# Kernel tuning notes

Measured on AMD Instinct MI355X. Metric: run time of the kernel, lower is better.

Reference implementation:

```python
import jax, jax.numpy as jnp
import numpy as np

D, H, DFF, DC = 1024, 16, 4096, 768
DH = D // H
EPS = 1e-5

def layer_norm(x, g, b):
    m = jnp.mean(x, axis=-1, keepdims=True)
    v = jnp.mean(jnp.square(x - m), axis=-1, keepdims=True)
    return (x - m) * jax.lax.rsqrt(v + EPS) * g + b

def setup_inputs() -> dict:
    key = jax.random.key(0)
    ks = jax.random.split(key, 20)
    s = 0.02
    return {
        "x": jax.random.normal(ks[0], (2, 2048, D), jnp.float32),
        "cond": jax.random.normal(ks[1], (2, 77, DC), jnp.float32),
        # self-attention params
        "Wqkv": jax.random.normal(ks[2], (D, 3 * D), jnp.float32) * s,
        "Wproj_sa": jax.random.normal(ks[3], (D, D), jnp.float32) * s,
        "bproj_sa": jnp.zeros((D,), jnp.float32),
        "g1": jnp.ones((D,), jnp.float32),
        "b1": jnp.zeros((D,), jnp.float32),
        # cross-attention params
        "Wq_ca": jax.random.normal(ks[4], (D, D), jnp.float32) * s,
        "Wkv_ca": jax.random.normal(ks[5], (DC, 2 * D), jnp.float32) * s,
        "Wproj_ca": jax.random.normal(ks[6], (D, D), jnp.float32) * s,
        "bproj_ca": jnp.zeros((D,), jnp.float32),
        "g2": jnp.ones((D,), jnp.float32),
        "b2": jnp.zeros((D,), jnp.float32),
        # feed-forward params
        "Wff1": jax.random.normal(ks[7], (D, DFF), jnp.float32) * s,
        "bff1": jnp.zeros((DFF,), jnp.float32),
        "Wff2": jax.random.normal(ks[8], (DFF, D), jnp.float32) * s,
        "bff2": jnp.zeros((D,), jnp.float32),
        "g3": jnp.ones((D,), jnp.float32),
        "b3": jnp.zeros((D,), jnp.float32),
    }

def _self_attn(x, Wqkv, Wproj, bproj):
    B, T, _ = x.shape
    qkv = x @ Wqkv                                   # (B,T,3D)
    qkv = qkv.reshape(B, T, 3, H, DH)
    q, k, v = (qkv[:, :, i].transpose(0, 2, 1, 3) for i in range(3))  # (B,H,T,DH)
    scale = DH ** -0.5
    attn = jnp.einsum('bhtd,bhsd->bhts', q, k) * scale  # (B,H,T,T)
    causal = jnp.triu(jnp.ones((T, T), bool), k=1)
    attn = jnp.where(causal, -jnp.inf, attn)
    attn = jax.nn.softmax(attn, axis=-1)
    out = jnp.einsum('bhts,bhsd->bhtd', attn, v)
    out = out.transpose(0, 2, 1, 3).reshape(B, T, D)
    return out @ Wproj + bproj

def _cross_attn(x, cond, Wq, Wkv, Wproj, bproj):
    B, T, _ = x.shape
    C = cond.shape[1]
    q = (x @ Wq).reshape(B, T, H, DH).transpose(0, 2, 1, 3)      # (B,H,T,DH)
    kv = (cond @ Wkv).reshape(B, C, 2, H, DH)
    k = kv[:, :, 0].transpose(0, 2, 1, 3)                         # (B,H,C,DH)
    v = kv[:, :, 1].transpose(0, 2, 1, 3)
    scale = DH ** -0.5
    attn = jax.nn.softmax(jnp.einsum('bhtd,bhcd->bhtc', q, k) * scale, axis=-1)
    out = jnp.einsum('bhtc,bhcd->bhtd', attn, v)
    out = out.transpose(0, 2, 1, 3).reshape(B, T, D)
    return out @ Wproj + bproj

def reference(x, cond, Wqkv, Wproj_sa, bproj_sa, g1, b1,
              Wq_ca, Wkv_ca, Wproj_ca, bproj_ca, g2, b2,
              Wff1, bff1, Wff2, bff2, g3, b3):
    x = x + _self_attn(layer_norm(x, g1, b1), Wqkv, Wproj_sa, bproj_sa)
    x = x + _cross_attn(layer_norm(x, g2, b2), cond, Wq_ca, Wkv_ca, Wproj_ca, bproj_ca)
    h = layer_norm(x, g3, b3)
    h = jax.nn.gelu(h @ Wff1 + bff1, approximate=False) @ Wff2 + bff2
    return x + h
```

## Files before the change

kernel.cpp:

```cpp
#include <hip/hip_runtime.h>

using bf16   = __bf16;
using bf16x8 = __attribute__((ext_vector_type(8))) bf16;
using bf16x4 = __attribute__((ext_vector_type(4))) bf16;
using f32x4  = __attribute__((ext_vector_type(4))) float;

#define DEV static __device__ __forceinline__

DEV void MFMA16(bf16x8 a, bf16x8 b, f32x4& c){
  c = __builtin_amdgcn_mfma_f32_16x16x32_bf16(a, b, c, 0, 0, 0);
}

DEV void gload16(const bf16* g, bf16* lds){
  __builtin_amdgcn_global_load_lds(
      (const __attribute__((address_space(1))) void*)g,
      (__attribute__((address_space(3))) void*)lds, 16, 0, 0);
}

DEV void tcast4_dev(const float* __restrict__ in, bf16* __restrict__ out,
                    int R, int C, int bx, int by, float scale, int nscale,
                    int tid, float (*t)[129])
{
  const int c0 = bx*128, r0 = by*32;
  #pragma unroll
  for (int i = 0; i < 4; ++i){
    int row = i*8 + (tid >> 5);
    int col = (tid & 31) * 4;
    const float4 v = *(const float4*)&in[(size_t)(r0+row)*C + c0 + col];
    t[row][col+0]=v.x; t[row][col+1]=v.y; t[row][col+2]=v.z; t[row][col+3]=v.w;
  }
  __syncthreads();
  const int c = tid >> 1, rh = (tid & 1) * 16;
  const float sc = (c0 + c < nscale) ? scale : 1.f;
  bf16 tmp[16];
  #pragma unroll
  for (int j = 0; j < 16; ++j) tmp[j] = (bf16)(t[rh+j][c] * sc);
  bf16* o = out + (size_t)(c0+c)*R + r0 + rh;
  *(bf16x8*)o       = *(bf16x8*)&tmp[0];
  *(bf16x8*)(o + 8) = *(bf16x8*)&tmp[8];
}

DEV void ln_dev(const float* __restrict__ x, const float* __restrict__ gw,
                const float* __restrict__ bw, bf16* __restrict__ y,
                int row, int tid, float (*red)[4])
{
  const float4 v = ((const float4*)(x + (size_t)row*1024))[tid];
  float s  = v.x+v.y+v.z+v.w;
  float s2 = v.x*v.x+v.y*v.y+v.z*v.z+v.w*v.w;
  #pragma unroll
  for (int off=32; off>=1; off>>=1){ s += __shfl_down(s,off); s2 += __shfl_down(s2,off); }
  const int wid = tid>>6, lane = tid&63;
  if (lane==0){ red[0][wid]=s; red[1][wid]=s2; }
  __syncthreads();
  s  = red[0][0]+red[0][1]+red[0][2]+red[0][3];
  s2 = red[1][0]+red[1][1]+red[1][2]+red[1][3];
  const float m  = s*(1.f/1024.f);
  const float rs = rsqrtf(s2*(1.f/1024.f) - m*m + 1e-5f);
  const float4 gv = ((const float4*)gw)[tid];
  const float4 bv = ((const float4*)bw)[tid];
  bf16* yr = y + (size_t)row*1024 + tid*4;
  yr[0] = (bf16)((v.x-m)*rs*gv.x + bv.x);
  yr[1] = (bf16)((v.y-m)*rs*gv.y + bv.y);
  yr[2] = (bf16)((v.z-m)*rs*gv.z + bv.z);
  yr[3] = (bf16)((v.w-m)*rs*gv.w + bv.w);
}

__global__ __launch_bounds__(256) void prep_ln(
    const float* Wqkv, bf16* wqkvT, const float* Wps, bf16* wpsT,
    const float* Wqc, bf16* wqcT, const float* Wkvc, bf16* wkvcT,
    const float* Wpc, bf16* wpcT, const float* Wf1, bf16* wf1T,
    const float* Wf2, bf16* wf2T, const float* cond, bf16* condb,
    const float* x, const float* g1, const float* b1, bf16* xn)
{
  __shared__ float t[32][129];
  __shared__ float red[2][4];
  const int bid = blockIdx.x, tid = threadIdx.x;
  if      (bid <  768) tcast4_dev(Wqkv, wqkvT, 1024, 3072, bid%24,        bid/24,        0.125f, 1024, tid, t);
  else if (bid < 1024) tcast4_dev(Wps,  wpsT,  1024, 1024, (bid-768)%8,   (bid-768)/8,   1.f, 0, tid, t);
  else if (bid < 1280) tcast4_dev(Wqc,  wqcT,  1024, 1024, (bid-1024)%8,  (bid-1024)/8,  0.125f, 1024, tid, t);
  else if (bid < 1664) tcast4_dev(Wkvc, wkvcT,  768, 2048, (bid-1280)%16, (bid-1280)/16, 1.f, 0, tid, t);
  else if (bid < 1920) tcast4_dev(Wpc,  wpcT,  1024, 1024, (bid-1664)%8,  (bid-1664)/8,  1.f, 0, tid, t);
  else if (bid < 2944) tcast4_dev(Wf1,  wf1T,  1024, 4096, (bid-1920)%32, (bid-1920)/32, 1.f, 0, tid, t);
  else if (bid < 3968) tcast4_dev(Wf2,  wf2T,  4096, 1024, (bid-2944)%8,  (bid-2944)/8,  1.f, 0, tid, t);
  else if (bid < 4084) {
    int i = (bid-3968)*256 + tid;
    if (i < 29568) {
      const float4 v = ((const float4*)cond)[i];
      bf16 o[4] = {(bf16)v.x,(bf16)v.y,(bf16)v.z,(bf16)v.w};
      *(bf16x4*)&condb[i*4] = *(bf16x4*)o;
    }
  } else {
    ln_dev(x, g1, b1, xn, bid - 4084, tid, red);
  }
}

__global__ __launch_bounds__(256) void ln_kernel(const float* __restrict__ x,
    const float* __restrict__ gw, const float* __restrict__ bw, bf16* __restrict__ y)
{
  __shared__ float red[2][4];
  ln_dev(x, gw, bw, y, blockIdx.x, threadIdx.x, red);
}

__global__ __launch_bounds__(256) void ln_re(
    const float* __restrict__ x1, const float* __restrict__ g2,
    const float* __restrict__ b2, bf16* __restrict__ xn,
    const bf16* __restrict__ kvca, bf16* __restrict__ kpad, bf16* __restrict__ vtca)
{
  __shared__ float red[2][4];
  const int bid = blockIdx.x, tid = threadIdx.x;
  if (bid < 4096) {
    ln_dev(x1, g2, b2, xn, bid, tid, red);
  } else {
    int idx = (bid - 4096)*256 + tid;
    int d = idx & 63, s = (idx>>6) & 127, h = (idx>>13) & 15, b = idx>>17;
    bf16 kv = (bf16)0.f, vv = (bf16)0.f;
    if (s < 77) {
      kv = kvca[(size_t)(b*77+s)*2048 + h*64 + d];
      vv = kvca[(size_t)(b*77+s)*2048 + 1024 + h*64 + d];
    }
    kpad[idx] = kv;
    vtca[(((size_t)(b*16+h)*64 + d)<<7) + s] = vv;
  }
}

template<int MODE>
__global__ __launch_bounds__(512) void gemm256p(
    const bf16* __restrict__ A, const bf16* __restrict__ Bt,
    const float* __restrict__ bias, const float* resid,
    void* outp, int M, int N, int K)
{
  __shared__ __align__(16) bf16 As[2][256*64];
  __shared__ __align__(16) bf16 Bs[2][256*64];
  const int tid = threadIdx.x;
  const int lane = tid & 63, wid = tid >> 6;
  const int l15 = lane & 15, lh = lane >> 4;
  const int wm = wid >> 2, wn = wid & 3;

  const int nwg = gridDim.x * gridDim.y;
  const int lin = blockIdx.y * gridDim.x + blockIdx.x;
  const int wg  = (lin & 7) * (nwg >> 3) + (lin >> 3);
  const size_t m0 = (size_t)(wg / gridDim.x) * 256;
  const size_t n0 = (size_t)(wg % gridDim.x) * 256;

  f32x4 acc[8][4];
  #pragma unroll
  for (int i=0;i<8;++i)
    #pragma unroll
    for (int j=0;j<4;++j) acc[i][j] = (f32x4){0.f,0.f,0.f,0.f};

  const int srow8 = lane >> 3;
  const int scol  = ((lane & 7) ^ srow8) * 8;
  const int NT = K >> 6;

  auto stageH = [&](int t, int j){
    if (t >= NT) return;
    const int k0 = t << 6;
    const int buf = t & 1;
    const int hl = j & 1;
    const bf16* src = (j < 2) ? A : Bt;
    const size_t base = (j < 2) ? m0 : n0;
    bf16* dst = (j < 2) ? &As[buf][0] : &Bs[buf][0];
    #pragma unroll
    for (int i = 0; i < 2; ++i) {
      int r = hl*128 + wid*16 + i*8;
      gload16(src + (base + (size_t)(r + srow8))*K + k0 + scol, dst + r*64);
    }
  };
  auto rdA = [&](int buf, int mh, int kk, bf16x8* dst){
    #pragma unroll
    for (int i=0;i<4;++i){
      int row = wm*128 + (mh*4+i)*16 + l15;
      dst[i] = *(const bf16x8*)&As[buf][row*64 + (((kk*4+lh) ^ (row&7))<<3)];
    }
  };
  auto rdB = [&](int buf, int kk, bf16x8* dst){
    #pragma unroll
    for (int n=0;n<4;++n){
      int row = wn*64 + n*16 + l15;
      dst[n] = *(const bf16x8*)&Bs[buf][row*64 + (((kk*4+lh) ^ (row&7))<<3)];
    }
  };

  stageH(0,0); stageH(0,1); stageH(0,2); stageH(0,3);
  stageH(1,0); stageH(1,1);
  if (NT > 1) asm volatile("s_waitcnt vmcnt(4)" ::: "memory");
  else        asm volatile("s_waitcnt vmcnt(0)" ::: "memory");
  __builtin_amdgcn_sched_barrier(0);
  __builtin_amdgcn_s_barrier();

  for (int t = 0; t < NT; ++t) {
    const int buf = t & 1;
    bf16x8 af0k0[4], af0k1[4], af1k0[4], af1k1[4], bfr0[4], bfr1[4];
    rdA(buf,0,0,af0k0); rdA(buf,0,1,af0k1); rdB(buf,0,bfr0);
    stageH(t+1,2);
    __builtin_amdgcn_s_barrier();
    asm volatile("s_waitcnt lgkmcnt(0)" ::: "memory");
    __builtin_amdgcn_sched_barrier(0);
    __builtin_amdgcn_s_setprio(1);
    #pragma unroll
    for (int mi=0;mi<4;++mi)
      #pragma unroll
      for (int ni=0;ni<4;++ni) MFMA16(af0k0[mi], bfr0[ni], acc[mi][ni]);
    __builtin_amdgcn_s_setprio(0);
    __builtin_amdgcn_sched_barrier(0);
    __builtin_amdgcn_s_barrier();
    rdA(buf,1,0,af1k0); rdA(buf,1,1,af1k1); rdB(buf,1,bfr1);
    stageH(t+1,3);
    __builtin_amdgcn_s_barrier();
    asm volatile("s_waitcnt lgkmcnt(0)" ::: "memory");
    __builtin_amdgcn_sched_barrier(0);
    __builtin_amdgcn_s_setprio(1);
    #pragma unroll
    for (int mi=0;mi<4;++mi)
      #pragma unroll
      for (int ni=0;ni<4;++ni) MFMA16(af1k0[mi], bfr0[ni], acc[4+mi][ni]);
    __builtin_amdgcn_s_setprio(0);
    __builtin_amdgcn_sched_barrier(0);
    __builtin_amdgcn_s_barrier();
    stageH(t+2,0);
    stageH(t+2,1);
    __builtin_amdgcn_s_setprio(1);
    #pragma unroll
    for (int mi=0;mi<4;++mi)
      #pragma unroll
      for (int ni=0;ni<4;++ni) MFMA16(af0k1[mi], bfr1[ni], acc[mi][ni]);
    #pragma unroll
    for (int mi=0;mi<4;++mi)
      #pragma unroll
      for (int ni=0;ni<4;++ni) MFMA16(af1k1[mi], bfr1[ni], acc[4+mi][ni]);
    __builtin_amdgcn_s_setprio(0);
    if (t + 2 < NT) asm volatile("s_waitcnt vmcnt(4)" ::: "memory");
    else            asm volatile("s_waitcnt vmcnt(0)" ::: "memory");
    __builtin_amdgcn_sched_barrier(0);
    __builtin_amdgcn_s_barrier();
  }

  #pragma unroll
  for (int mi=0;mi<8;++mi){
    #pragma unroll
    for (int r=0;r<4;++r){
      size_t row = m0 + wm*128 + mi*16 + 4*lh + r;
      #pragma unroll
      for (int ni=0;ni<4;++ni){
        size_t col = n0 + wn*64 + ni*16 + l15;
        float v = acc[mi][ni][r];
        if (MODE==0) ((bf16*)outp)[row*(size_t)N + col] = (bf16)v;
        else if (MODE==1) ((float*)outp)[row*(size_t)N + col] = v + bias[col] + resid[row*(size_t)N + col];
        else { v += bias[col];
               ((bf16*)outp)[row*(size_t)N + col] =
                   (bf16)(0.5f*v*(1.0f + erff(v*0.70710678f))); }
      }
    }
  }
}

DEV void g32_body(bf16* As, bf16* Bs, size_t m0, size_t n0,
                  const bf16* __restrict__ A, const bf16* __restrict__ Bt,
                  const float* __restrict__ bias, const float* resid,
                  void* outp, int M, int N, int K, int mode, int tid)
{
  const int lane = tid & 63, wid = tid >> 6;
  const int l15 = lane & 15, lh = lane >> 4;

  f32x4 acc[2][2];
  #pragma unroll
  for (int i=0;i<2;++i)
    #pragma unroll
    for (int j=0;j<2;++j) acc[i][j] = (f32x4){0.f,0.f,0.f,0.f};

  const int srow8 = lane >> 3;
  const int scol  = ((lane & 7) ^ srow8) * 8;
  const int NT = K >> 6;

  auto stage = [&](int t, int buf){
    const int k0 = t << 6;
    {
      int r = wid*8;
      int ar = (int)m0 + r + srow8; if (ar >= M) ar = M - 1;
      gload16(A + (size_t)ar*K + k0 + scol, As + buf*2048 + r*64);
    }
    #pragma unroll
    for (int i = 0; i < 4; ++i) {
      int r = wid*32 + i*8;
      gload16(Bt + (n0 + (size_t)(r + srow8))*K + k0 + scol, Bs + buf*8192 + r*64);
    }
  };

  stage(0, 0);
  __syncthreads();

  for (int t = 0; t < NT; ++t) {
    const int cur = t & 1;
    if (t + 1 < NT) stage(t + 1, cur ^ 1);
    #pragma unroll
    for (int kk = 0; kk < 2; ++kk) {
      bf16x8 af[2], bfr[2];
      #pragma unroll
      for (int i=0;i<2;++i){
        const int arow = i*16 + l15;
        af[i]  = *(const bf16x8*)&As[cur*2048 + arow*64 + (((kk*4+lh) ^ (arow&7))<<3)];
      }
      #pragma unroll
      for (int n=0;n<2;++n){
        const int brow = wid*32 + n*16 + l15;
        bfr[n] = *(const bf16x8*)&Bs[cur*8192 + brow*64 + (((kk*4+lh) ^ (brow&7))<<3)];
      }
      #pragma unroll
      for (int mi=0;mi<2;++mi)
        #pragma unroll
        for (int ni=0;ni<2;++ni)
          MFMA16(af[mi], bfr[ni], acc[mi][ni]);
    }
    __syncthreads();
  }

  #pragma unroll
  for (int mi=0;mi<2;++mi){
    #pragma unroll
    for (int r=0;r<4;++r){
      size_t row = m0 + mi*16 + 4*lh + r;
      if (row < (size_t)M) {
        #pragma unroll
        for (int ni=0;ni<2;++ni){
          size_t col = n0 + wid*32 + ni*16 + l15;
          float v = acc[mi][ni][r];
          if (mode == 0) ((bf16*)outp)[row*(size_t)N + col] = (bf16)v;
          else ((float*)outp)[row*(size_t)N + col] = v + bias[col] + resid[row*(size_t)N + col];
        }
      }
    }
  }
}

template<int MODE>
__global__ __launch_bounds__(256) void gemm32(
    const bf16* __restrict__ A, const bf16* __restrict__ Bt,
    const float* __restrict__ bias, const float* resid,
    void* outp, int M, int N, int K)
{
  __shared__ __align__(16) bf16 As[2*32*64];
  __shared__ __align__(16) bf16 Bs[2*128*64];
  const int nwg = gridDim.x * gridDim.y;
  const int lin = blockIdx.y * gridDim.x + blockIdx.x;
  const int wg  = (lin & 7) * (nwg >> 3) + (lin >> 3);
  const size_t m0 = (size_t)(wg / gridDim.x) * 32;
  const size_t n0 = (size_t)(wg % gridDim.x) * 128;
  g32_body(As, Bs, m0, n0, A, Bt, bias, resid, outp, M, N, K, MODE, threadIdx.x);
}

__global__ __launch_bounds__(256) void proj_kv(
    const bf16* __restrict__ attn, const bf16* __restrict__ wprojSaT,
    const float* __restrict__ bproj, const float* __restrict__ x, float* x1,
    const bf16* __restrict__ condb, const bf16* __restrict__ wkvCaT, bf16* kvca)
{
  __shared__ __align__(16) bf16 As[2*32*64];
  __shared__ __align__(16) bf16 Bs[2*128*64];
  const int bid = blockIdx.x;
  if (bid < 1024) {
    const int wg  = (bid & 7) * 128 + (bid >> 3);
    const size_t m0 = (size_t)(wg >> 3) * 32;
    const size_t n0 = (size_t)(wg & 7) * 128;
    g32_body(As, Bs, m0, n0, attn, wprojSaT, bproj, x, x1,
             4096, 1024, 1024, 1, threadIdx.x);
  } else {
    const int g = bid - 1024;
    const size_t m0 = (size_t)(g / 16) * 32;
    const size_t n0 = (size_t)(g % 16) * 128;
    g32_body(As, Bs, m0, n0, condb, wkvCaT, nullptr, nullptr, kvca,
             154, 2048, 768, 0, threadIdx.x);
  }
}

__global__ __launch_bounds__(256) void vtsa_kernel(const bf16* __restrict__ qkv, bf16* __restrict__ vt)
{
  __shared__ bf16 t[32][33];
  const int b = blockIdx.z >> 4, h = blockIdx.z & 15;
  const int s0 = blockIdx.x*32, d0 = blockIdx.y*32;
  const int tx = threadIdx.x & 31, ty = threadIdx.x >> 5;
  #pragma unroll
  for (int i = ty; i < 32; i += 8)
    t[i][tx] = qkv[(size_t)(b*2048 + s0+i)*3072 + 2048 + h*64 + d0 + tx];
  __syncthreads();
  #pragma unroll
  for (int i = ty; i < 32; i += 8)
    vt[((size_t)blockIdx.z*64 + d0+i)*2048 + s0 + tx] = t[tx][i];
}

template<int CAUSAL>
__global__ __launch_bounds__(256) void flash6(
    const bf16* __restrict__ qb, long q_bstride, long qstride,
    const bf16* __restrict__ kb0, long k_bstride, long k_hstride, long kstride,
    const bf16* __restrict__ vtb, long vt_bhstride, long vtstride,
    bf16* __restrict__ out, int skv)
{
  __shared__ __align__(16) bf16 Ks[2][64*64];
  __shared__ __align__(16) bf16 Vs[2][64*64];
  __shared__ __align__(16) bf16 Ps[4][16*68];
  const int tid = threadIdx.x;
  const int w = tid >> 6, lane = tid & 63, l15 = lane & 15, lh = lane >> 4;
  const int bid = blockIdx.x;
  const int bh   = (bid & 7) + 8*((bid >> 3) & 3);
  const int tile = 31 - (bid >> 5);
  const int b = bh >> 4, h = bh & 15;
  const int q0 = tile * 64;
  const int nkb   = CAUSAL ? tile + 1 : ((skv + 63) >> 6);
  const int nfull = CAUSAL ? tile     : (skv >> 6);

  const bf16* kbase = kb0 + (size_t)b*k_bstride + (size_t)h*k_hstride;
  const bf16* vbase = vtb + (size_t)bh*vt_bhstride;
  const int sr0 = tid >> 3, sslot = tid & 7;

  const bf16* qrow = qb + (size_t)b*q_bstride + (size_t)h*64
                        + (size_t)(q0 + w*16 + l15)*qstride;
  bf16x8 qf0 = *(const bf16x8*)(qrow + 8*lh);
  bf16x8 qf1 = *(const bf16x8*)(qrow + 32 + 8*lh);

  f32x4 o[4];
  #pragma unroll
  for (int i=0;i<4;++i) o[i] = (f32x4){0.f,0.f,0.f,0.f};
  float lacc[4] = {0.f,0.f,0.f,0.f};

  bf16x8 kreg[2], vreg[2];
  #pragma unroll
  for (int i=0;i<2;++i){
    int r = sr0 + 32*i;
    kreg[i] = *(const bf16x8*)(kbase + (size_t)r*kstride + sslot*8);
    vreg[i] = *(const bf16x8*)(vbase + (size_t)r*vtstride + sslot*8);
  }

  for (int kb = 0; kb < nkb; ++kb) {
    const int buf = kb & 1;
    #pragma unroll
    for (int i=0;i<2;++i){
      int r = sr0 + 32*i;
      int ps = (sslot ^ (r & 7)) * 8;
      *(bf16x8*)&Ks[buf][r*64 + ps] = kreg[i];
      *(bf16x8*)&Vs[buf][r*64 + ps] = vreg[i];
    }
    __syncthreads();
    if (kb + 1 < nkb) {
      #pragma unroll
      for (int i=0;i<2;++i){
        int r = sr0 + 32*i;
        kreg[i] = *(const bf16x8*)(kbase + (size_t)((kb+1)*64 + r)*kstride + sslot*8);
        vreg[i] = *(const bf16x8*)(vbase + (size_t)r*vtstride + (kb+1)*64 + sslot*8);
      }
    }
    f32x4 sf[4];
    __builtin_amdgcn_s_setprio(1);
    #pragma unroll
    for (int ni = 0; ni < 4; ++ni) {
      int kr = ni*16 + l15;
      bf16x8 kf0 = *(const bf16x8*)&Ks[buf][kr*64 + (((lh  ) ^ (kr&7))<<3)];
      bf16x8 kf1 = *(const bf16x8*)&Ks[buf][kr*64 + (((lh+4) ^ (kr&7))<<3)];
      f32x4 z = (f32x4){0.f,0.f,0.f,0.f};
      MFMA16(qf0, kf0, z);
      MFMA16(qf1, kf1, z);
      sf[ni] = z;
    }
    __builtin_amdgcn_s_setprio(0);
    if (kb >= nfull) {
      #pragma unroll
      for (int ni=0;ni<4;++ni){
        int col = kb*64 + ni*16 + l15;
        #pragma unroll
        for (int r=0;r<4;++r){
          int rowg = q0 + w*16 + 4*lh + r;
          if (col >= skv || (CAUSAL && col > rowg)) sf[ni][r] = -1e30f;
        }
      }
    }
    #pragma unroll
    for (int ni=0;ni<4;++ni){
      #pragma unroll
      for (int r=0;r<4;++r){
        float p = __expf(sf[ni][r]);
        lacc[r] += p;
        Ps[w][(4*lh + r)*68 + ni*16 + l15] = (bf16)p;
      }
    }
    bf16x8 pa0 = *(const bf16x8*)&Ps[w][l15*68 + 8*lh];
    bf16x8 pa1 = *(const bf16x8*)&Ps[w][l15*68 + 32 + 8*lh];
    __builtin_amdgcn_s_setprio(1);
    #pragma unroll
    for (int nd=0;nd<4;++nd){
      int vr = nd*16 + l15;
      bf16x8 vf0 = *(const bf16x8*)&Vs[buf][vr*64 + (((lh  ) ^ (vr&7))<<3)];
      bf16x8 vf1 = *(const bf16x8*)&Vs[buf][vr*64 + (((lh+4) ^ (vr&7))<<3)];
      MFMA16(pa0, vf0, o[nd]);
      MFMA16(pa1, vf1, o[nd]);
    }
    __builtin_amdgcn_s_setprio(0);
  }
  float lr[4];
  #pragma unroll
  for (int r=0;r<4;++r) lr[r] = lacc[r];
  #pragma unroll
  for (int off=1; off<16; off<<=1)
    #pragma unroll
    for (int r=0;r<4;++r) lr[r] += __shfl_xor(lr[r], off);
  #pragma unroll
  for (int nd=0;nd<4;++nd)
    #pragma unroll
    for (int r=0;r<4;++r){
      int rowg = q0 + w*16 + 4*lh + r;
      out[(size_t)(b*2048 + rowg)*1024 + h*64 + nd*16 + l15] =
          (bf16)(o[nd][r] / lr[r]);
    }
}

struct Bump { char* base; size_t off;
  void* get(size_t bytes){ void* p = base + off; off += (bytes + 255) & ~(size_t)255; return p; } };

extern "C" void kernel_launch(void* const* d_in, const int* in_sizes, int n_in,
                              void* d_out, int out_size, void* d_ws, size_t ws_size,
                              hipStream_t stream)
{
  const float* x        = (const float*)d_in[0];
  const float* cond     = (const float*)d_in[1];
  const float* Wqkv     = (const float*)d_in[2];
  const float* Wproj_sa = (const float*)d_in[3];
  const float* bproj_sa = (const float*)d_in[4];
  const float* g1       = (const float*)d_in[5];
  const float* b1       = (const float*)d_in[6];
  const float* Wq_ca    = (const float*)d_in[7];
  const float* Wkv_ca   = (const float*)d_in[8];
  const float* Wproj_ca = (const float*)d_in[9];
  const float* bproj_ca = (const float*)d_in[10];
  const float* g2       = (const float*)d_in[11];
  const float* b2       = (const float*)d_in[12];
  const float* Wff1     = (const float*)d_in[13];
  const float* bff1     = (const float*)d_in[14];
  const float* Wff2     = (const float*)d_in[15];
  const float* bff2     = (const float*)d_in[16];
  const float* g3       = (const float*)d_in[17];
  const float* b3       = (const float*)d_in[18];

  Bump bump{(char*)d_ws, 0};
  bf16* wqkvT    = (bf16*)bump.get((size_t)3072*1024*2);
  bf16* wprojSaT = (bf16*)bump.get((size_t)1024*1024*2);
  bf16* wqCaT    = (bf16*)bump.get((size_t)1024*1024*2);
  bf16* wkvCaT   = (bf16*)bump.get((size_t)2048*768*2);
  bf16* wprojCaT = (bf16*)bump.get((size_t)1024*1024*2);
  bf16* wff1T    = (bf16*)bump.get((size_t)4096*1024*2);
  bf16* wff2T    = (bf16*)bump.get((size_t)1024*4096*2);
  bf16* condb    = (bf16*)bump.get((size_t)154*768*2);
  bf16* xn       = (bf16*)bump.get((size_t)4096*1024*2);
  bf16* qkv      = (bf16*)bump.get((size_t)4096*3072*2);
  bf16* vt_sa    = (bf16*)bump.get((size_t)2*16*64*2048*2);
  bf16* attn     = (bf16*)bump.get((size_t)4096*1024*2);
  bf16* kvca     = (bf16*)bump.get((size_t)154*2048*2);
  bf16* kpad     = (bf16*)bump.get((size_t)2*16*128*64*2);
  bf16* vtca     = (bf16*)bump.get((size_t)2*16*64*128*2);
  bf16* h1   = qkv;
  bf16* qca  = vt_sa;
  float* x1  = (float*)d_out;

  prep_ln<<<dim3(8180), 256, 0, stream>>>(
      Wqkv, wqkvT, Wproj_sa, wprojSaT, Wq_ca, wqCaT, Wkv_ca, wkvCaT,
      Wproj_ca, wprojCaT, Wff1, wff1T, Wff2, wff2T, cond, condb,
      x, g1, b1, xn);

  gemm256p<0><<<dim3(12,16), 512, 0, stream>>>(xn, wqkvT, nullptr, nullptr, qkv, 4096, 3072, 1024);
  vtsa_kernel<<<dim3(64,2,32), 256, 0, stream>>>(qkv, vt_sa);
  flash6<1><<<dim3(1024), 256, 0, stream>>>(
      qkv,        (long)2048*3072, 3072,
      qkv + 1024, (long)2048*3072, 64, 3072,
      vt_sa,      (long)64*2048, 2048,
      attn, 2048);
  proj_kv<<<dim3(1104), 256, 0, stream>>>(attn, wprojSaT, bproj_sa, x, x1,
                                          condb, wkvCaT, kvca);

  ln_re<<<dim3(5120), 256, 0, stream>>>(x1, g2, b2, xn, kvca, kpad, vtca);
  gemm32<0><<<dim3(8,128), 256, 0, stream>>>(xn, wqCaT, nullptr, nullptr, qca, 4096, 1024, 1024);
  flash6<0><<<dim3(1024), 256, 0, stream>>>(
      qca,  (long)2048*1024, 1024,
      kpad, (long)16*128*64, (long)128*64, 64,
      vtca, (long)64*128, 128,
      attn, 77);
  gemm32<1><<<dim3(8,128), 256, 0, stream>>>(attn, wprojCaT, bproj_ca, x1, x1, 4096, 1024, 1024);

  ln_kernel<<<dim3(4096), 256, 0, stream>>>(x1, g3, b3, xn);
  gemm256p<2><<<dim3(16,16), 512, 0, stream>>>(xn, wff1T, bff1, nullptr, h1, 4096, 4096, 1024);
  gemm32<1><<<dim3(8,128), 256, 0, stream>>>(h1, wff2T, bff2, x1, d_out, 4096, 1024, 4096);

  (void)in_sizes; (void)n_in; (void)out_size; (void)ws_size;
}
```

Measured before the change: 296.1 us.

## Split-K the FF2 GEMM with 128x128 tiles and a partial-sum reduction

The final FF2 projection (4096x1024, K=4096) moves from a 32-row-tile GEMM to a new 128x128-tile kernel split into two K halves. The first half writes bias plus residual plus partial result directly to the output, the second half writes to a float workspace, and a separate kernel adds the two. This aims at better data reuse from larger tiles while keeping enough blocks (512) to fill the GPU. The cost is an extra 16MB fp32 write and read and one more kernel launch.

```diff
diff --git a/kernel.cpp b/kernel.cpp
--- a/kernel.cpp
+++ b/kernel.cpp
@@ -252,6 +252,111 @@
       }
     }
   }
+}
+
+DEV void gbt_body(bf16* As, bf16* Bs, size_t m0, size_t n0,
+                  const bf16* __restrict__ A, const bf16* __restrict__ Bt,
+                  const float* __restrict__ bias, const float* resid,
+                  void* outp, int M, int N, int KLEN, int LDK, int mode, int tid)
+{
+  const int lane = tid & 63, wid = tid >> 6;
+  const int l15 = lane & 15, lh = lane >> 4;
+  const int wm = wid >> 1, wn = wid & 1;
+
+  f32x4 acc[4][4];
+  #pragma unroll
+  for (int i=0;i<4;++i)
+    #pragma unroll
+    for (int j=0;j<4;++j) acc[i][j] = (f32x4){0.f,0.f,0.f,0.f};
+
+  const int srow8 = lane >> 3;
+  const int scol  = ((lane & 7) ^ srow8) * 8;
+  const int NT = KLEN >> 6;
+
+  auto stage = [&](int t, int buf){
+    const int k0 = t << 6;
+    #pragma unroll
+    for (int i = 0; i < 4; ++i) {
+      int r = wid*32 + i*8;
+      int ar = (int)m0 + r + srow8; if (ar >= M) ar = M - 1;
+      gload16(A  + (size_t)ar*LDK + k0 + scol,                   As + buf*8192 + r*64);
+      gload16(Bt + (n0 + (size_t)(r + srow8))*LDK + k0 + scol,   Bs + buf*8192 + r*64);
+    }
+  };
+
+  stage(0, 0);
+  __syncthreads();
+
+  for (int t = 0; t < NT; ++t) {
+    const int cur = t & 1;
+    if (t + 1 < NT) stage(t + 1, cur ^ 1);
+    #pragma unroll
+    for (int kk = 0; kk < 2; ++kk) {
+      bf16x8 af[4], bfr[4];
+      #pragma unroll
+      for (int i=0;i<4;++i){
+        const int arow = wm*64 + i*16 + l15;
+        const int brow = wn*64 + i*16 + l15;
+        af[i]  = *(const bf16x8*)&As[cur*8192 + arow*64 + (((kk*4+lh) ^ (arow&7))<<3)];
+        bfr[i] = *(const bf16x8*)&Bs[cur*8192 + brow*64 + (((kk*4+lh) ^ (brow&7))<<3)];
+      }
+      #pragma unroll
+      for (int mi=0;mi<4;++mi)
+        #pragma unroll
+        for (int ni=0;ni<4;++ni)
+          MFMA16(af[mi], bfr[ni], acc[mi][ni]);
+    }
+    __syncthreads();
+  }
+
+  #pragma unroll
+  for (int mi=0;mi<4;++mi){
+    #pragma unroll
+    for (int r=0;r<4;++r){
+      size_t row = m0 + wm*64 + mi*16 + 4*lh + r;
+      if (row < (size_t)M) {
+        #pragma unroll
+        for (int ni=0;ni<4;++ni){
+          size_t col = n0 + wn*64 + ni*16 + l15;
+          float v = acc[mi][ni][r];
+          if (mode == 1) ((float*)outp)[row*(size_t)N + col] = v + bias[col] + resid[row*(size_t)N + col];
+          else           ((float*)outp)[row*(size_t)N + col] = v;
+        }
+      }
+    }
+  }
+}
+
+__global__ __launch_bounds__(256) void ff2_split(
+    const bf16* __restrict__ h1, const bf16* __restrict__ wff2T,
+    const float* __restrict__ bff2, const float* __restrict__ x1,
+    float* dout, float* part)
+{
+  __shared__ __align__(16) bf16 As[2*128*64];
+  __shared__ __align__(16) bf16 Bs[2*128*64];
+  const int bid = blockIdx.x;
+  const int split = bid >> 8;
+  const int g = bid & 255;
+  const int wg = (g & 7) * 32 + (g >> 3);
+  const size_t m0 = (size_t)(wg >> 3) * 128;
+  const size_t n0 = (size_t)(wg & 7) * 128;
+  const int kb = split * 2048;
+  if (split == 0)
+    gbt_body(As, Bs, m0, n0, h1 + kb, wff2T + kb, bff2, x1, dout,
+             4096, 1024, 2048, 4096, 1, threadIdx.x);
+  else
+    gbt_body(As, Bs, m0, n0, h1 + kb, wff2T + kb, nullptr, nullptr, part,
+             4096, 1024, 2048, 4096, 3, threadIdx.x);
+}
+
+__global__ __launch_bounds__(256) void addpart(float* __restrict__ dout,
+                                               const float* __restrict__ part)
+{
+  size_t i = ((size_t)blockIdx.x*256 + threadIdx.x) * 4;
+  float4 a = *(float4*)&dout[i];
+  const float4 b = *(const float4*)&part[i];
+  a.x += b.x; a.y += b.y; a.z += b.z; a.w += b.w;
+  *(float4*)&dout[i] = a;
 }
 
 DEV void g32_body(bf16* As, bf16* Bs, size_t m0, size_t n0,
@@ -552,6 +657,7 @@
   bf16* kvca     = (bf16*)bump.get((size_t)154*2048*2);
   bf16* kpad     = (bf16*)bump.get((size_t)2*16*128*64*2);
   bf16* vtca     = (bf16*)bump.get((size_t)2*16*64*128*2);
+  float* part    = (float*)bump.get((size_t)4096*1024*4);
   bf16* h1   = qkv;
   bf16* qca  = vt_sa;
   float* x1  = (float*)d_out;
@@ -582,7 +688,8 @@
 
   ln_kernel<<<dim3(4096), 256, 0, stream>>>(x1, g3, b3, xn);
   gemm256p<2><<<dim3(16,16), 512, 0, stream>>>(xn, wff1T, bff1, nullptr, h1, 4096, 4096, 1024);
-  gemm32<1><<<dim3(8,128), 256, 0, stream>>>(h1, wff2T, bff2, x1, d_out, 4096, 1024, 4096);
+  ff2_split<<<dim3(512), 256, 0, stream>>>(h1, wff2T, bff2, x1, (float*)d_out, part);
+  addpart<<<dim3(4096), 256, 0, stream>>>((float*)d_out, part);
 
   (void)in_sizes; (void)n_in; (void)out_size; (void)ws_size;
 }
```

After: 302.8 us. +2.3%, slower.
